# Kernel optimization log

Hardware: AMD Instinct MI355X
Metric: run time of the kernel (lower is better)

## Reference

```python
import jax, jax.numpy as jnp
import numpy as np

NEG_SLOPE = 0.2  # DenseGATConv default negative_slope


def _add_self_loops(adj):
    n = adj.shape[-1]
    idx = jnp.arange(n)
    return adj.at[:, idx, idx].set(1.0)


def dense_gat_conv(x, adj, W, att_src, att_dst, bias, concat):
    """PyG DenseGATConv forward (eval mode, add_loop=True).
    x: [B,N,F], adj: [B,N,N] (0/1), W: [F,H*C], att_*: [H,C], bias: [H*C] or [C]."""
    B, N, _ = x.shape
    H, C = att_src.shape
    h = (x @ W).reshape(B, N, H, C)                     # projected features
    a_src = jnp.einsum('bnhc,hc->bnh', h, att_src)      # [B,N,H]
    a_dst = jnp.einsum('bnhc,hc->bnh', h, att_dst)      # [B,N,H]
    # alpha[b,i,j,h] = a_src[b,j,h] + a_dst[b,i,h]
    alpha = a_src[:, None, :, :] + a_dst[:, :, None, :]  # [B,N,N,H]
    alpha = jax.nn.leaky_relu(alpha, NEG_SLOPE)
    adj = _add_self_loops(adj)
    alpha = jnp.where(adj[..., None] == 0, -jnp.inf, alpha)
    alpha = jax.nn.softmax(alpha, axis=2)               # softmax over sources j
    out = jnp.einsum('bijh,bjhc->bihc', alpha, h)       # [B,N,H,C]
    out = out.reshape(B, N, H * C) if concat else out.mean(axis=2)
    return out + bias


def setup_inputs() -> dict:
    key = jax.random.key(0)
    ks = jax.random.split(key, 10)
    B, N, F, H, C, NC = 1, 4096, 512, 8, 64, 16
    x = jax.random.normal(ks[0], (B, N, F), dtype=jnp.float32)
    adj = (jax.random.uniform(ks[1], (B, N, N)) < 0.01).astype(jnp.float32)
    s1 = 1.0 / np.sqrt(F)
    s2 = 1.0 / np.sqrt(H * C)
    return {
        'x': x,
        'adj': adj,
        'W1': jax.random.normal(ks[2], (F, H * C), dtype=jnp.float32) * s1,
        'att_src1': jax.random.normal(ks[3], (H, C), dtype=jnp.float32) * s1,
        'att_dst1': jax.random.normal(ks[4], (H, C), dtype=jnp.float32) * s1,
        'b1': jnp.zeros((H * C,), dtype=jnp.float32),
        'W2': jax.random.normal(ks[5], (H * C, NC), dtype=jnp.float32) * s2,
        'att_src2': jax.random.normal(ks[6], (1, NC), dtype=jnp.float32) * s2,
        'att_dst2': jax.random.normal(ks[7], (1, NC), dtype=jnp.float32) * s2,
        'b2': jnp.zeros((NC,), dtype=jnp.float32),
    }


def reference(x, adj, W1, att_src1, att_dst1, b1, W2, att_src2, att_dst2, b2):
    # eval mode: all dropout(p=0.6) layers are identity
    h = dense_gat_conv(x, adj, W1, att_src1, att_dst1, b1, concat=True)
    h = jax.nn.elu(h)
    out = dense_gat_conv(h, adj, W2, att_src2, att_dst2, b2, concat=False)
    return out
```

## Files before the change

kernel.cpp:

```cpp
#include <hip/hip_runtime.h>
#include <hip/hip_bf16.h>
#include <hip/hip_fp16.h>

#define N_NODES 4096
#define F_IN    512
#define HC      512
#define H_HEADS 8
#define C_DIM   64
#define NCLS    16
#define CAP     192
#define NEG_SLOPE 0.2f

typedef __bf16 bf16x8 __attribute__((ext_vector_type(8)));
typedef float  f32x4  __attribute__((ext_vector_type(4)));
typedef unsigned short us8 __attribute__((ext_vector_type(8)));

#define GBLKS 512


__global__ __launch_bounds__(256) void k_gemm1(const float* __restrict__ x,
                                               const float* __restrict__ W1,
                                               const float* __restrict__ att_src,
                                               const float* __restrict__ att_dst,
                                               const float* __restrict__ adj,
                                               __half* __restrict__ C,
                                               float* __restrict__ a_src,
                                               float* __restrict__ a_dst,
                                               int* __restrict__ row_cnt,
                                               int* __restrict__ col_idx) {
    __shared__ __align__(16) ushort sAhi[2048], sAlo[2048], sBhi[2048], sBlo[2048];
    __shared__ float s_s[2][64], s_d[2][64];
    __shared__ int cnt_s;
    int b = blockIdx.x;
    int t = threadIdx.x;
    if (b >= GBLKS) {
        int i = b - GBLKS;
        if (t == 0) cnt_s = 0;
        __syncthreads();
        const float4* row = (const float4*)(adj + (size_t)i * N_NODES);
        int* cols = col_idx + (size_t)i * CAP;
#pragma unroll
        for (int it = 0; it < 4; ++it) {
            int idx4 = it * 256 + t;
            float4 v = row[idx4];
            int j0 = idx4 * 4;
            if (v.x != 0.f && j0 + 0 != i) { int p = atomicAdd(&cnt_s, 1); if (p < CAP - 1) cols[p] = j0 + 0; }
            if (v.y != 0.f && j0 + 1 != i) { int p = atomicAdd(&cnt_s, 1); if (p < CAP - 1) cols[p] = j0 + 1; }
            if (v.z != 0.f && j0 + 2 != i) { int p = atomicAdd(&cnt_s, 1); if (p < CAP - 1) cols[p] = j0 + 2; }
            if (v.w != 0.f && j0 + 3 != i) { int p = atomicAdd(&cnt_s, 1); if (p < CAP - 1) cols[p] = j0 + 3; }
        }
        __syncthreads();
        if (t == 0) {
            int p = min(cnt_s, CAP - 1);
            cols[p] = i;
            row_cnt[i] = p + 1;
        }
        return;
    }
    int w = t >> 6, lane = t & 63;
    int head = b >> 6;
    int n0 = head * 64;
    int m0 = (b & 63) * 64;
    int mw = (w & 1) * 32, nw = (w >> 1) * 32;
    int g0 = (w & 1) * 2;
    bool isB = (w >> 1) != 0;
    f32x4 acc[2][2] = {};
    for (int kb = 0; kb < 16; ++kb) {
#pragma unroll
        for (int gg = 0; gg < 2; ++gg) {
            int g  = g0 + gg;
            int rn = (isB ? n0 : m0) + g * 16 + (lane & 15);
            int kk = kb * 32 + (lane >> 4) * 8;
            float f[8];
            if (!isB) {
                float4 v0 = *(const float4*)&x[(size_t)rn * F_IN + kk];
                float4 v1 = *(const float4*)&x[(size_t)rn * F_IN + kk + 4];
                f[0] = v0.x; f[1] = v0.y; f[2] = v0.z; f[3] = v0.w;
                f[4] = v1.x; f[5] = v1.y; f[6] = v1.z; f[7] = v1.w;
            } else {
#pragma unroll
                for (int u = 0; u < 8; ++u) f[u] = W1[(size_t)(kk + u) * HC + rn];
            }
            us8 hv, lv;
#pragma unroll
            for (int u = 0; u < 8; ++u) {
                __bf16 h = (__bf16)f[u];
                __bf16 lo_ = (__bf16)(f[u] - (float)h);
                hv[u] = __builtin_bit_cast(unsigned short, h);
                lv[u] = __builtin_bit_cast(unsigned short, lo_);
            }
            ushort* dh = isB ? sBhi : sAhi;
            ushort* dl = isB ? sBlo : sAlo;
            *(us8*)&dh[g * 512 + lane * 8] = hv;
            *(us8*)&dl[g * 512 + lane * 8] = lv;
        }
        __syncthreads();
        bf16x8 ahi[2], alo[2], bhi[2], blo[2];
#pragma unroll
        for (int mi = 0; mi < 2; ++mi) {
            int g = (mw >> 4) + mi;
            ahi[mi] = __builtin_bit_cast(bf16x8, *(const us8*)&sAhi[g * 512 + lane * 8]);
            alo[mi] = __builtin_bit_cast(bf16x8, *(const us8*)&sAlo[g * 512 + lane * 8]);
        }
#pragma unroll
        for (int ni = 0; ni < 2; ++ni) {
            int g = (nw >> 4) + ni;
            bhi[ni] = __builtin_bit_cast(bf16x8, *(const us8*)&sBhi[g * 512 + lane * 8]);
            blo[ni] = __builtin_bit_cast(bf16x8, *(const us8*)&sBlo[g * 512 + lane * 8]);
        }
#pragma unroll
        for (int mi = 0; mi < 2; ++mi)
#pragma unroll
            for (int ni = 0; ni < 2; ++ni) {
                acc[mi][ni] = __builtin_amdgcn_mfma_f32_16x16x32_bf16(ahi[mi], bhi[ni], acc[mi][ni], 0, 0, 0);
                acc[mi][ni] = __builtin_amdgcn_mfma_f32_16x16x32_bf16(alo[mi], bhi[ni], acc[mi][ni], 0, 0, 0);
                acc[mi][ni] = __builtin_amdgcn_mfma_f32_16x16x32_bf16(ahi[mi], blo[ni], acc[mi][ni], 0, 0, 0);
            }
        __syncthreads();
    }
    int r0 = (lane >> 4) * 4;
    int cn = lane & 15;
    float as0 = att_src[n0 + nw + cn],      as1 = att_src[n0 + nw + 16 + cn];
    float ad0 = att_dst[n0 + nw + cn],      ad1 = att_dst[n0 + nw + 16 + cn];
#pragma unroll
    for (int mi = 0; mi < 2; ++mi)
#pragma unroll
        for (int r = 0; r < 4; ++r) {
            float ps = acc[mi][0][r] * as0 + acc[mi][1][r] * as1;
            float pd = acc[mi][0][r] * ad0 + acc[mi][1][r] * ad1;
#pragma unroll
            for (int o = 1; o < 16; o <<= 1) {
                ps += __shfl_xor(ps, o, 64);
                pd += __shfl_xor(pd, o, 64);
            }
            if (cn == 0) {
                int row = mw + mi * 16 + r0 + r;
                s_s[w >> 1][row] = ps;
                s_d[w >> 1][row] = pd;
            }
        }
#pragma unroll
    for (int mi = 0; mi < 2; ++mi)
#pragma unroll
        for (int ni = 0; ni < 2; ++ni) {
            size_t base = (size_t)(m0 + mw + mi * 16 + r0) * HC + (n0 + nw + ni * 16 + cn);
#pragma unroll
            for (int r = 0; r < 4; ++r)
                C[base + (size_t)r * HC] = __float2half(acc[mi][ni][r]);
        }
    __syncthreads();
    if (t < 64) {
        a_src[(m0 + t) * H_HEADS + head] = s_s[0][t] + s_s[1][t];
        a_dst[(m0 + t) * H_HEADS + head] = s_d[0][t] + s_d[1][t];
    }
}

__global__ __launch_bounds__(256) void k_agg1(const __half* __restrict__ hf,
                                              const float* __restrict__ a_src,
                                              const float* __restrict__ a_dst,
                                              const int* __restrict__ row_cnt,
                                              const int* __restrict__ col_idx,
                                              const float* __restrict__ b1,
                                              const float* __restrict__ W2,
                                              const float* __restrict__ att_src2,
                                              const float* __restrict__ att_dst2,
                                              float* __restrict__ h2,
                                              float* __restrict__ a_src2,
                                              float* __restrict__ a_dst2) {
    int i = blockIdx.x;
    int t = threadIdx.x;
    __shared__ float wL[CAP][H_HEADS];
    __shared__ int   colL[CAP];
    __shared__ float denom[H_HEADS];
    __shared__ float ad[H_HEADS];
    __shared__ float elu_s[HC];
    __shared__ float part[16][17];
    int cnt = row_cnt[i];
    if (t < H_HEADS) ad[t] = a_dst[i * H_HEADS + t];
    for (int j = t; j < cnt; j += 256) colL[j] = col_idx[(size_t)i * CAP + j];
    __syncthreads();
    for (int idx = t; idx < cnt * H_HEADS; idx += 256) {
        int j = idx >> 3, h = idx & 7;
        float l = a_src[colL[j] * H_HEADS + h] + ad[h];
        l = (l > 0.f) ? l : NEG_SLOPE * l;
        wL[j][h] = __expf(l);
    }
    __syncthreads();
    {
        int h = t >> 5, l32 = t & 31;
        float s = 0.f;
        for (int j = l32; j < cnt; j += 32) s += wL[j][h];
#pragma unroll
        for (int o = 16; o > 0; o >>= 1) s += __shfl_down(s, o, 32);
        if (l32 == 0) denom[h] = s;
    }
    __syncthreads();
    int e = t * 2;
    int h = e >> 6;
    float ax = 0.f, ay = 0.f;
    int j = 0;
    for (; j + 8 <= cnt; j += 8) {
        int c0 = colL[j],     c1 = colL[j + 1], c2 = colL[j + 2], c3 = colL[j + 3];
        int c4 = colL[j + 4], c5 = colL[j + 5], c6 = colL[j + 6], c7 = colL[j + 7];
        float2 v0 = __half22float2(*(const __half2*)&hf[(size_t)c0 * HC + e]);
        float2 v1 = __half22float2(*(const __half2*)&hf[(size_t)c1 * HC + e]);
        float2 v2 = __half22float2(*(const __half2*)&hf[(size_t)c2 * HC + e]);
        float2 v3 = __half22float2(*(const __half2*)&hf[(size_t)c3 * HC + e]);
        float2 v4 = __half22float2(*(const __half2*)&hf[(size_t)c4 * HC + e]);
        float2 v5 = __half22float2(*(const __half2*)&hf[(size_t)c5 * HC + e]);
        float2 v6 = __half22float2(*(const __half2*)&hf[(size_t)c6 * HC + e]);
        float2 v7 = __half22float2(*(const __half2*)&hf[(size_t)c7 * HC + e]);
        float w0 = wL[j][h],     w1 = wL[j + 1][h], w2 = wL[j + 2][h], w3 = wL[j + 3][h];
        float w4 = wL[j + 4][h], w5 = wL[j + 5][h], w6 = wL[j + 6][h], w7 = wL[j + 7][h];
        ax += w0 * v0.x + w1 * v1.x + w2 * v2.x + w3 * v3.x
            + w4 * v4.x + w5 * v5.x + w6 * v6.x + w7 * v7.x;
        ay += w0 * v0.y + w1 * v1.y + w2 * v2.y + w3 * v3.y
            + w4 * v4.y + w5 * v5.y + w6 * v6.y + w7 * v7.y;
    }
    for (; j + 4 <= cnt; j += 4) {
        int c0 = colL[j], c1 = colL[j + 1], c2 = colL[j + 2], c3 = colL[j + 3];
        float2 v0 = __half22float2(*(const __half2*)&hf[(size_t)c0 * HC + e]);
        float2 v1 = __half22float2(*(const __half2*)&hf[(size_t)c1 * HC + e]);
        float2 v2 = __half22float2(*(const __half2*)&hf[(size_t)c2 * HC + e]);
        float2 v3 = __half22float2(*(const __half2*)&hf[(size_t)c3 * HC + e]);
        float w0 = wL[j][h], w1 = wL[j + 1][h], w2 = wL[j + 2][h], w3 = wL[j + 3][h];
        ax += w0 * v0.x + w1 * v1.x + w2 * v2.x + w3 * v3.x;
        ay += w0 * v0.y + w1 * v1.y + w2 * v2.y + w3 * v3.y;
    }
    for (; j < cnt; ++j) {
        int c0 = colL[j];
        float2 v0 = __half22float2(*(const __half2*)&hf[(size_t)c0 * HC + e]);
        float w0 = wL[j][h];
        ax += w0 * v0.x;
        ay += w0 * v0.y;
    }
    float inv = 1.f / denom[h];
    float o0 = ax * inv + b1[e];
    float o1 = ay * inv + b1[e + 1];
    o0 = (o0 > 0.f) ? o0 : (__expf(o0) - 1.f);
    o1 = (o1 > 0.f) ? o1 : (__expf(o1) - 1.f);
    elu_s[e]     = o0;
    elu_s[e + 1] = o1;
    __syncthreads();
    int kg = t >> 4, c = t & 15;
    float p = 0.f;
    const float* w2p = W2 + (size_t)kg * 32 * NCLS + c;
    const float* es  = &elu_s[kg * 32];
#pragma unroll 8
    for (int kk = 0; kk < 32; ++kk) p += es[kk] * w2p[kk * NCLS];
    part[kg][c] = p;
    __syncthreads();
    if (t < 16) {
        float s = 0.f;
#pragma unroll
        for (int r = 0; r < 16; ++r) s += part[r][t];
        h2[(size_t)i * NCLS + t] = s;
        float vs = s * att_src2[t], vd = s * att_dst2[t];
#pragma unroll
        for (int o = 8; o > 0; o >>= 1) {
            vs += __shfl_xor(vs, o, 64);
            vd += __shfl_xor(vd, o, 64);
        }
        if (t == 0) { a_src2[i] = vs; a_dst2[i] = vd; }
    }
}

__global__ __launch_bounds__(256) void k_agg2(const float* __restrict__ h2,
                                              const float* __restrict__ a_src2,
                                              const float* __restrict__ a_dst2,
                                              const int* __restrict__ row_cnt,
                                              const int* __restrict__ col_idx,
                                              const float* __restrict__ b2,
                                              float* __restrict__ out) {
    int t = threadIdx.x;
    int w = t >> 6, lane = t & 63;
    int i = blockIdx.x * 4 + w;
    __shared__ float ew[4][CAP];
    __shared__ int   colL[4][CAP];
    int cnt = row_cnt[i];
    float adi = a_dst2[i];
    float sum = 0.f;
    for (int j = lane; j < cnt; j += 64) {
        int col = col_idx[(size_t)i * CAP + j];
        colL[w][j] = col;
        float l = a_src2[col] + adi;
        l = (l > 0.f) ? l : NEG_SLOPE * l;
        float e = __expf(l);
        ew[w][j] = e;
        sum += e;
    }
#pragma unroll
    for (int o = 32; o > 0; o >>= 1) sum += __shfl_xor(sum, o, 64);
    int q = lane >> 4, c = lane & 15;
    float acc = 0.f;
    for (int j = q; j < cnt; j += 4)
        acc += ew[w][j] * h2[(size_t)colL[w][j] * NCLS + c];
    acc += __shfl_down(acc, 32, 64);
    acc += __shfl_down(acc, 16, 64);
    if (lane < NCLS)
        out[(size_t)i * NCLS + lane] = acc / sum + b2[lane];
}

extern "C" void kernel_launch(void* const* d_in, const int* in_sizes, int n_in,
                              void* d_out, int out_size, void* d_ws, size_t ws_size,
                              hipStream_t stream) {
    const float* x        = (const float*)d_in[0];
    const float* adj      = (const float*)d_in[1];
    const float* W1       = (const float*)d_in[2];
    const float* att_src1 = (const float*)d_in[3];
    const float* att_dst1 = (const float*)d_in[4];
    const float* b1       = (const float*)d_in[5];
    const float* W2       = (const float*)d_in[6];
    const float* att_src2 = (const float*)d_in[7];
    const float* att_dst2 = (const float*)d_in[8];
    const float* b2       = (const float*)d_in[9];
    float* out = (float*)d_out;

    char* ws = (char*)d_ws;
    int*    row_cnt = (int*)ws;     ws += (size_t)N_NODES * 4;
    int*    col_idx = (int*)ws;     ws += (size_t)N_NODES * CAP * 4;
    __half* h1f     = (__half*)ws;  ws += (size_t)N_NODES * HC * 2;
    float*  a_src   = (float*)ws;   ws += (size_t)N_NODES * H_HEADS * 4;
    float*  a_dst   = (float*)ws;   ws += (size_t)N_NODES * H_HEADS * 4;
    float*  h2      = (float*)ws;   ws += (size_t)N_NODES * NCLS * 4;
    float*  as2     = (float*)ws;   ws += (size_t)N_NODES * 4;
    float*  ad2     = (float*)ws;   ws += (size_t)N_NODES * 4;

    hipLaunchKernelGGL(k_gemm1, dim3(GBLKS + N_NODES), dim3(256), 0, stream,
                       x, W1, att_src1, att_dst1, adj,
                       h1f, a_src, a_dst, row_cnt, col_idx);
    hipLaunchKernelGGL(k_agg1, dim3(N_NODES), dim3(256), 0, stream,
                       h1f, a_src, a_dst, row_cnt, col_idx, b1,
                       W2, att_src2, att_dst2, h2, as2, ad2);
    hipLaunchKernelGGL(k_agg2, dim3(N_NODES / 4), dim3(256), 0, stream,
                       h2, as2, ad2, row_cnt, col_idx, b2, out);
}
```

Baseline: 160.6 us.

## Pre-split W1 into bf16 hi/lo tiles and enlarge GEMM M-tile to 128

Adds a small kernel that converts W1 once into transposed bf16 hi/lo fragments laid out for the MFMA tiles. The GEMM then streams those fragments into LDS with direct global-to-LDS loads instead of doing strided per-element W1 reads and the split inside every block. The GEMM block tile also doubles along M (128x64), halving the number of GEMM blocks and the redundant B loads while each wave holds more accumulators. The cost is an extra launch, more workspace, and higher register and LDS use per block.

```diff
diff --git a/kernel.cpp b/kernel.cpp
--- a/kernel.cpp
+++ b/kernel.cpp
@@ -15,11 +15,49 @@
 typedef float  f32x4  __attribute__((ext_vector_type(4)));
 typedef unsigned short us8 __attribute__((ext_vector_type(8)));
 
-#define GBLKS 512
-
+#define GT 256
+
+
+__global__ __launch_bounds__(256) void k_wsplit(const float* __restrict__ W,
+                                                ushort* __restrict__ whiT,
+                                                ushort* __restrict__ wloT) {
+    __shared__ float tile[64][65];
+    int bb = blockIdx.x;
+    int t = threadIdx.x;
+    int n0 = (bb & 7) * 64, k0 = (bb >> 3) * 64;
+#pragma unroll
+    for (int i = 0; i < 4; ++i) {
+        int r = i * 16 + (t >> 4);
+        int c = (t & 15) * 4;
+        *(float4*)&tile[r][c] = *(const float4*)&W[(size_t)(k0 + r) * HC + n0 + c];
+    }
+    __syncthreads();
+    int rg_local = t >> 6;
+    int l = t & 63;
+    int n_local = rg_local * 16 + (l & 15);
+#pragma unroll
+    for (int kb_local = 0; kb_local < 2; ++kb_local) {
+        int k_local = kb_local * 32 + (l >> 4) * 8;
+        us8 hv, lv;
+#pragma unroll
+        for (int u = 0; u < 8; ++u) {
+            float f = tile[k_local + u][n_local];
+            __bf16 h = (__bf16)f;
+            __bf16 lo_ = (__bf16)(f - (float)h);
+            hv[u] = __builtin_bit_cast(unsigned short, h);
+            lv[u] = __builtin_bit_cast(unsigned short, lo_);
+        }
+        int rg = (n0 >> 4) + rg_local;
+        int kb = (k0 >> 5) + kb_local;
+        size_t off = ((size_t)(rg * 16 + kb) * 64 + l) * 8;
+        *(us8*)&whiT[off] = hv;
+        *(us8*)&wloT[off] = lv;
+    }
+}
 
 __global__ __launch_bounds__(256) void k_gemm1(const float* __restrict__ x,
-                                               const float* __restrict__ W1,
+                                               const ushort* __restrict__ Bhi,
+                                               const ushort* __restrict__ Blo,
                                                const float* __restrict__ att_src,
                                                const float* __restrict__ att_dst,
                                                const float* __restrict__ adj,
@@ -28,13 +66,13 @@
                                                float* __restrict__ a_dst,
                                                int* __restrict__ row_cnt,
                                                int* __restrict__ col_idx) {
-    __shared__ __align__(16) ushort sAhi[2048], sAlo[2048], sBhi[2048], sBlo[2048];
-    __shared__ float s_s[2][64], s_d[2][64];
+    __shared__ __align__(16) ushort sAhi[4096], sAlo[4096], sBhi[2048], sBlo[2048];
+    __shared__ float s_s[2][128], s_d[2][128];
     __shared__ int cnt_s;
     int b = blockIdx.x;
     int t = threadIdx.x;
-    if (b >= GBLKS) {
-        int i = b - GBLKS;
+    if (b >= GT) {
+        int i = b - GT;
         if (t == 0) cnt_s = 0;
         __syncthreads();
         const float4* row = (const float4*)(adj + (size_t)i * N_NODES);
@@ -58,29 +96,30 @@
         return;
     }
     int w = t >> 6, lane = t & 63;
-    int head = b >> 6;
+    int head = b >> 5;
     int n0 = head * 64;
-    int m0 = (b & 63) * 64;
-    int mw = (w & 1) * 32, nw = (w >> 1) * 32;
-    int g0 = (w & 1) * 2;
-    bool isB = (w >> 1) != 0;
-    f32x4 acc[2][2] = {};
+    int m0 = (b & 31) * 128;
+    int mh = w & 1, nh = w >> 1;
+    f32x4 acc[4][2] = {};
     for (int kb = 0; kb < 16; ++kb) {
+        {
+            size_t off = ((size_t)((head * 4 + w) * 16 + kb) * 64 + lane) * 8;
+            __builtin_amdgcn_global_load_lds(
+                (const __attribute__((address_space(1))) void*)(Bhi + off),
+                (__attribute__((address_space(3))) void*)&sBhi[w * 512], 16, 0, 0);
+            __builtin_amdgcn_global_load_lds(
+                (const __attribute__((address_space(1))) void*)(Blo + off),
+                (__attribute__((address_space(3))) void*)&sBlo[w * 512], 16, 0, 0);
+        }
 #pragma unroll
         for (int gg = 0; gg < 2; ++gg) {
-            int g  = g0 + gg;
-            int rn = (isB ? n0 : m0) + g * 16 + (lane & 15);
+            int g = 2 * w + gg;
+            int row = m0 + g * 16 + (lane & 15);
             int kk = kb * 32 + (lane >> 4) * 8;
-            float f[8];
-            if (!isB) {
-                float4 v0 = *(const float4*)&x[(size_t)rn * F_IN + kk];
-                float4 v1 = *(const float4*)&x[(size_t)rn * F_IN + kk + 4];
-                f[0] = v0.x; f[1] = v0.y; f[2] = v0.z; f[3] = v0.w;
-                f[4] = v1.x; f[5] = v1.y; f[6] = v1.z; f[7] = v1.w;
-            } else {
-#pragma unroll
-                for (int u = 0; u < 8; ++u) f[u] = W1[(size_t)(kk + u) * HC + rn];
-            }
+            const float* src = &x[(size_t)row * F_IN + kk];
+            float4 v0 = *(const float4*)&src[0];
+            float4 v1 = *(const float4*)&src[4];
+            float f[8] = {v0.x, v0.y, v0.z, v0.w, v1.x, v1.y, v1.z, v1.w};
             us8 hv, lv;
 #pragma unroll
             for (int u = 0; u < 8; ++u) {
@@ -89,27 +128,25 @@
                 hv[u] = __builtin_bit_cast(unsigned short, h);
                 lv[u] = __builtin_bit_cast(unsigned short, lo_);
             }
-            ushort* dh = isB ? sBhi : sAhi;
-            ushort* dl = isB ? sBlo : sAlo;
-            *(us8*)&dh[g * 512 + lane * 8] = hv;
-            *(us8*)&dl[g * 512 + lane * 8] = lv;
+            *(us8*)&sAhi[g * 512 + lane * 8] = hv;
+            *(us8*)&sAlo[g * 512 + lane * 8] = lv;
         }
         __syncthreads();
-        bf16x8 ahi[2], alo[2], bhi[2], blo[2];
-#pragma unroll
-        for (int mi = 0; mi < 2; ++mi) {
-            int g = (mw >> 4) + mi;
+        bf16x8 ahi[4], alo[4], bhi[2], blo[2];
+#pragma unroll
+        for (int mi = 0; mi < 4; ++mi) {
+            int g = mh * 4 + mi;
             ahi[mi] = __builtin_bit_cast(bf16x8, *(const us8*)&sAhi[g * 512 + lane * 8]);
             alo[mi] = __builtin_bit_cast(bf16x8, *(const us8*)&sAlo[g * 512 + lane * 8]);
         }
 #pragma unroll
         for (int ni = 0; ni < 2; ++ni) {
-            int g = (nw >> 4) + ni;
+            int g = nh * 2 + ni;
             bhi[ni] = __builtin_bit_cast(bf16x8, *(const us8*)&sBhi[g * 512 + lane * 8]);
             blo[ni] = __builtin_bit_cast(bf16x8, *(const us8*)&sBlo[g * 512 + lane * 8]);
         }
 #pragma unroll
-        for (int mi = 0; mi < 2; ++mi)
+        for (int mi = 0; mi < 4; ++mi)
 #pragma unroll
             for (int ni = 0; ni < 2; ++ni) {
                 acc[mi][ni] = __builtin_amdgcn_mfma_f32_16x16x32_bf16(ahi[mi], bhi[ni], acc[mi][ni], 0, 0, 0);
@@ -120,10 +157,10 @@
     }
     int r0 = (lane >> 4) * 4;
     int cn = lane & 15;
-    float as0 = att_src[n0 + nw + cn],      as1 = att_src[n0 + nw + 16 + cn];
-    float ad0 = att_dst[n0 + nw + cn],      ad1 = att_dst[n0 + nw + 16 + cn];
-#pragma unroll
-    for (int mi = 0; mi < 2; ++mi)
+    float as0 = att_src[n0 + nh * 32 + cn],      as1 = att_src[n0 + nh * 32 + 16 + cn];
+    float ad0 = att_dst[n0 + nh * 32 + cn],      ad1 = att_dst[n0 + nh * 32 + 16 + cn];
+#pragma unroll
+    for (int mi = 0; mi < 4; ++mi)
 #pragma unroll
         for (int r = 0; r < 4; ++r) {
             float ps = acc[mi][0][r] * as0 + acc[mi][1][r] * as1;
@@ -134,22 +171,22 @@
                 pd += __shfl_xor(pd, o, 64);
             }
             if (cn == 0) {
-                int row = mw + mi * 16 + r0 + r;
-                s_s[w >> 1][row] = ps;
-                s_d[w >> 1][row] = pd;
+                int row = mh * 64 + mi * 16 + r0 + r;
+                s_s[nh][row] = ps;
+                s_d[nh][row] = pd;
             }
         }
 #pragma unroll
-    for (int mi = 0; mi < 2; ++mi)
+    for (int mi = 0; mi < 4; ++mi)
 #pragma unroll
         for (int ni = 0; ni < 2; ++ni) {
-            size_t base = (size_t)(m0 + mw + mi * 16 + r0) * HC + (n0 + nw + ni * 16 + cn);
+            size_t base = (size_t)(m0 + mh * 64 + mi * 16 + r0) * HC + (n0 + nh * 32 + ni * 16 + cn);
 #pragma unroll
             for (int r = 0; r < 4; ++r)
                 C[base + (size_t)r * HC] = __float2half(acc[mi][ni][r]);
         }
     __syncthreads();
-    if (t < 64) {
+    if (t < 128) {
         a_src[(m0 + t) * H_HEADS + head] = s_s[0][t] + s_s[1][t];
         a_dst[(m0 + t) * H_HEADS + head] = s_d[0][t] + s_d[1][t];
     }
@@ -325,9 +362,12 @@
     float*  h2      = (float*)ws;   ws += (size_t)N_NODES * NCLS * 4;
     float*  as2     = (float*)ws;   ws += (size_t)N_NODES * 4;
     float*  ad2     = (float*)ws;   ws += (size_t)N_NODES * 4;
-
-    hipLaunchKernelGGL(k_gemm1, dim3(GBLKS + N_NODES), dim3(256), 0, stream,
-                       x, W1, att_src1, att_dst1, adj,
+    ushort* w_hiT   = (ushort*)ws;  ws += (size_t)F_IN * HC * 2;
+    ushort* w_loT   = (ushort*)ws;  ws += (size_t)F_IN * HC * 2;
+
+    hipLaunchKernelGGL(k_wsplit, dim3(64), dim3(256), 0, stream, W1, w_hiT, w_loT);
+    hipLaunchKernelGGL(k_gemm1, dim3(GT + N_NODES), dim3(256), 0, stream,
+                       x, w_hiT, w_loT, att_src1, att_dst1, adj,
                        h1f, a_src, a_dst, row_cnt, col_idx);
     hipLaunchKernelGGL(k_agg1, dim3(N_NODES), dim3(256), 0, stream,
                        h1f, a_src, a_dst, row_cnt, col_idx, b1,
```

New measurement: 160.7 us. Within noise of the previous version (+0.1%).
